# Performance work log

Hardware: AMD Instinct MI355X
Metric: run time of the kernel (lower is better)

The kernel has to match this reference:

```python
import jax, jax.numpy as jnp
import numpy as np

EPSILON = 0.1
ALPHA = 0.5
N_ITER = 10
B, N, D, N_USERS = 4096, 4096, 16, 100000


def setup_inputs() -> dict:
    key = jax.random.key(0)
    k1, k2, k3, k4, k5, k6 = jax.random.split(key, 6)
    users_tensor = jax.random.randint(k1, (B,), 0, N_USERS)
    pois_tensor = jax.random.randint(k2, (B, N), 0, N)
    D_tensor = jax.random.uniform(k3, (B, N), dtype=jnp.float32)
    # ScaledEmbedding: normal init scaled by 1/embedding_dim
    poi_emb = jax.random.normal(k4, (N, D), dtype=jnp.float32) / D
    user_emb = jax.random.normal(k5, (N_USERS, D), dtype=jnp.float32) / D
    capacities = jax.random.uniform(k6, (N,), dtype=jnp.float32) + 0.5
    return {"users_tensor": users_tensor, "pois_tensor": pois_tensor,
            "D_tensor": D_tensor, "poi_emb": poi_emb,
            "user_emb": user_emb, "capacities": capacities}


def reference(users_tensor, pois_tensor, D_tensor, poi_emb, user_emb, capacities):
    pe = poi_emb[pois_tensor]            # [B, N, D]
    ue = user_emb[users_tensor]          # [B, D]
    dot = jnp.einsum('bnd,bd->bn', pe, ue)   # [B, N]
    affinity = (1.0 - ALPHA) * dot - ALPHA * (D_tensor / jnp.mean(D_tensor))
    K = jnp.exp(affinity / EPSILON)      # [B, N]
    a = jnp.ones((B,), dtype=K.dtype)
    b = capacities

    def body(i, uv):
        u, v = uv
        u = a / (K @ v)        # [B]
        v = b / (K.T @ u)      # [N]
        return (u, v)

    u0 = jnp.ones((B,), dtype=K.dtype)
    v0 = jnp.ones((N,), dtype=K.dtype)
    u, v = jax.lax.fori_loop(0, N_ITER, body, (u0, v0))
    P = K * (u[:, None] * v[None, :])    # [B, N]
    return P
```

## Files before the change

### kernel.cpp

```cpp
#include <hip/hip_runtime.h>
#include <hip/hip_fp16.h>

#define BB 4096
#define NN 4096
#define RPB 4
#define RPI 8
#define NBLK (BB / RPI)

__device__ __forceinline__ int swz(int bid) { return (bid & 7) * 64 + (bid >> 3); }

__global__ __launch_bounds__(256) void k_mean(
        const float* __restrict__ Dt, float* __restrict__ dsum,
        float* __restrict__ v) {
    const int tid = blockIdx.x * blockDim.x + threadIdx.x;
    const int gs = gridDim.x * blockDim.x;
    if (tid < NN) v[tid] = 1.0f;
    const float4* D4 = (const float4*)Dt;
    const int total4 = (BB * NN) / 4;
    float s = 0.f;
    for (int i = tid; i < total4; i += gs) {
        float4 d = D4[i];
        s += (d.x + d.y) + (d.z + d.w);
    }
    #pragma unroll
    for (int off = 32; off > 0; off >>= 1) s += __shfl_down(s, off, 64);
    __shared__ float ls[4];
    if ((threadIdx.x & 63) == 0) ls[threadIdx.x >> 6] = s;
    __syncthreads();
    if (threadIdx.x == 0) atomicAdd(dsum, (ls[0] + ls[1]) + (ls[2] + ls[3]));
}

__global__ __launch_bounds__(256) void k_K(
        const int* __restrict__ users, const int* __restrict__ pois,
        const float* __restrict__ Dt, const float* __restrict__ poi_emb,
        const float* __restrict__ user_emb, const float* __restrict__ dsum,
        __half* __restrict__ K) {
    __shared__ __half slut[RPB][NN];
    __shared__ float ues[RPB * 16];
    const int t = threadIdx.x;
    const int b0 = blockIdx.x * RPB;
    if (t < RPB * 16) {
        int r = t >> 4, d = t & 15;
        ues[t] = user_emb[(size_t)users[b0 + r] * 16 + d];
    }
    __syncthreads();
    float ue[RPB][16];
    #pragma unroll
    for (int r = 0; r < RPB; r++)
        #pragma unroll
        for (int d = 0; d < 16; d++) ue[r][d] = ues[r * 16 + d];

    const float4* pe4 = (const float4*)poi_emb;
    for (int j = t; j < NN; j += 256) {
        float4 p0 = pe4[j * 4 + 0];
        float4 p1 = pe4[j * 4 + 1];
        float4 p2 = pe4[j * 4 + 2];
        float4 p3 = pe4[j * 4 + 3];
        #pragma unroll
        for (int r = 0; r < RPB; r++) {
            float acc = p0.x*ue[r][0]  + p0.y*ue[r][1]  + p0.z*ue[r][2]  + p0.w*ue[r][3]
                      + p1.x*ue[r][4]  + p1.y*ue[r][5]  + p1.z*ue[r][6]  + p1.w*ue[r][7]
                      + p2.x*ue[r][8]  + p2.y*ue[r][9]  + p2.z*ue[r][10] + p2.w*ue[r][11]
                      + p3.x*ue[r][12] + p3.y*ue[r][13] + p3.z*ue[r][14] + p3.w*ue[r][15];
            slut[r][j] = __float2half(acc);
        }
    }
    __syncthreads();
    const float cc = 5.0f * 16777216.0f / dsum[0];
    #pragma unroll
    for (int r = 0; r < RPB; r++) {
        const size_t base = (size_t)(b0 + r) * NN;
        const int4*   p4 = (const int4*)(pois + base);
        const float4* d4 = (const float4*)(Dt + base);
        #pragma unroll
        for (int i = 0; i < NN / 4 / 256; i++) {
            const int q = t + i * 256;
            int4   ci = p4[q];
            float4 cd = d4[q];
            float k0 = __expf(5.0f * __half2float(slut[r][ci.x]) - cc * cd.x);
            float k1 = __expf(5.0f * __half2float(slut[r][ci.y]) - cc * cd.y);
            float k2 = __expf(5.0f * __half2float(slut[r][ci.z]) - cc * cd.z);
            float k3 = __expf(5.0f * __half2float(slut[r][ci.w]) - cc * cd.w);
            __half2* kw = (__half2*)&K[base + 4 * (size_t)q];
            kw[0] = __floats2half2_rn(k0, k1);
            kw[1] = __floats2half2_rn(k2, k3);
        }
    }
}

__global__ __launch_bounds__(512) void k_it(
        const __half* __restrict__ K, const float* __restrict__ v,
        float* __restrict__ part, float* __restrict__ u) {
    const int t = threadIdx.x;
    const int sb = swz(blockIdx.x);
    const int r0 = sb * RPI;

    const float4* w4 = (const float4*)v;
    float4 w0 = w4[2 * t], w1 = w4[2 * t + 1];

    float4 h[RPI];
    #pragma unroll
    for (int r = 0; r < RPI; r++)
        h[r] = ((const float4*)(K + (size_t)(r0 + r) * NN))[t];

    float acc[RPI];
    #pragma unroll
    for (int r = 0; r < RPI; r++) {
        const __half2* a = (const __half2*)&h[r];
        float2 f; float s = 0.f;
        f = __half22float2(a[0]); s += f.x * w0.x + f.y * w0.y;
        f = __half22float2(a[1]); s += f.x * w0.z + f.y * w0.w;
        f = __half22float2(a[2]); s += f.x * w1.x + f.y * w1.y;
        f = __half22float2(a[3]); s += f.x * w1.z + f.y * w1.w;
        acc[r] = s;
    }
    #pragma unroll
    for (int off = 32; off > 0; off >>= 1)
        #pragma unroll
        for (int r = 0; r < RPI; r++) acc[r] += __shfl_down(acc[r], off, 64);
    __shared__ float ls[8][RPI];
    __shared__ float us[RPI];
    if ((t & 63) == 0)
        #pragma unroll
        for (int r = 0; r < RPI; r++) ls[t >> 6][r] = acc[r];
    __syncthreads();
    if (t < RPI) {
        float s = 0.f;
        #pragma unroll
        for (int wv = 0; wv < 8; wv++) s += ls[wv][t];
        float uu = 1.0f / s;
        us[t] = uu;
        u[r0 + t] = uu;
    }
    __syncthreads();

    float4 A0 = make_float4(0, 0, 0, 0), A1 = A0;
    #pragma unroll
    for (int r = 0; r < RPI; r++) {
        const float ur = us[r];
        const __half2* a = (const __half2*)&h[r];
        float2 f;
        f = __half22float2(a[0]); A0.x += ur * f.x; A0.y += ur * f.y;
        f = __half22float2(a[1]); A0.z += ur * f.x; A0.w += ur * f.y;
        f = __half22float2(a[2]); A1.x += ur * f.x; A1.y += ur * f.y;
        f = __half22float2(a[3]); A1.z += ur * f.x; A1.w += ur * f.y;
    }
    float4* p4 = (float4*)(part + (size_t)sb * NN);
    p4[2 * t]     = A0;
    p4[2 * t + 1] = A1;
}

__global__ __launch_bounds__(256) void k_red(
        const float* __restrict__ part, const float* __restrict__ cap,
        float* __restrict__ v) {
    const int t = threadIdx.x;
    const int g = blockIdx.x;
    const int j = t & 7;
    const int s = t >> 3;
    const float4* p4 = (const float4*)part;
    float4 a = make_float4(0, 0, 0, 0);
    #pragma unroll
    for (int i = 0; i < NBLK / 32; i++) {
        float4 x = p4[(size_t)(s + 32 * i) * (NN / 4) + g * 8 + j];
        a.x += x.x; a.y += x.y; a.z += x.z; a.w += x.w;
    }
    __shared__ float4 red[32][8];
    red[s][j] = a;
    __syncthreads();
    if (t < 8) {
        float4 b = red[0][t];
        #pragma unroll
        for (int s2 = 1; s2 < 32; s2++) {
            float4 x = red[s2][t];
            b.x += x.x; b.y += x.y; b.z += x.z; b.w += x.w;
        }
        float4 cc = ((const float4*)cap)[g * 8 + t];
        ((float4*)v)[g * 8 + t] =
            make_float4(cc.x / b.x, cc.y / b.y, cc.z / b.z, cc.w / b.w);
    }
}

__global__ __launch_bounds__(256) void k_P(
        const __half* __restrict__ K, const float* __restrict__ u,
        const float* __restrict__ v, float* __restrict__ P) {
    const int t = threadIdx.x;
    const int sb = swz(blockIdx.x);
    const int r0 = sb * RPI;
    const float4* v4 = (const float4*)v;
    float4 va0 = v4[2 * t],       va1 = v4[2 * t + 1];
    float4 vb0 = v4[512 + 2 * t], vb1 = v4[512 + 2 * t + 1];
    #pragma unroll 2
    for (int r = 0; r < RPI; r++) {
        const int b = r0 + r;
        const float ub = u[b];
        const size_t base = (size_t)b * NN;
        const float4* k4 = (const float4*)(K + base);
        float4 raw0 = k4[t], raw1 = k4[256 + t];
        const __half2* ha = (const __half2*)&raw0;
        const __half2* hb = (const __half2*)&raw1;
        float2 f0 = __half22float2(ha[0]);
        float2 f1 = __half22float2(ha[1]);
        float2 f2 = __half22float2(ha[2]);
        float2 f3 = __half22float2(ha[3]);
        float2 g0 = __half22float2(hb[0]);
        float2 g1 = __half22float2(hb[1]);
        float2 g2 = __half22float2(hb[2]);
        float2 g3 = __half22float2(hb[3]);
        float4* P4 = (float4*)(P + base);
        P4[2*t]       = make_float4(f0.x*ub*va0.x, f0.y*ub*va0.y, f1.x*ub*va0.z, f1.y*ub*va0.w);
        P4[2*t+1]     = make_float4(f2.x*ub*va1.x, f2.y*ub*va1.y, f3.x*ub*va1.z, f3.y*ub*va1.w);
        P4[512+2*t]   = make_float4(g0.x*ub*vb0.x, g0.y*ub*vb0.y, g1.x*ub*vb0.z, g1.y*ub*vb0.w);
        P4[512+2*t+1] = make_float4(g2.x*ub*vb1.x, g2.y*ub*vb1.y, g3.x*ub*vb1.z, g3.y*ub*vb1.w);
    }
}

extern "C" void kernel_launch(void* const* d_in, const int* in_sizes, int n_in,
                              void* d_out, int out_size, void* d_ws, size_t ws_size,
                              hipStream_t stream) {
    const int*   users    = (const int*)d_in[0];
    const int*   pois     = (const int*)d_in[1];
    const float* Dt       = (const float*)d_in[2];
    const float* poi_emb  = (const float*)d_in[3];
    const float* user_emb = (const float*)d_in[4];
    const float* cap      = (const float*)d_in[5];
    float* out = (float*)d_out;

    float*  wsf  = (float*)d_ws;
    float*  dsum = wsf;
    float*  u    = wsf + 64;
    float*  v    = wsf + 64 + BB;
    __half* Kh   = (__half*)(wsf + 64 + BB + NN);
    float*  part = (float*)d_out;

    hipMemsetAsync(dsum, 0, sizeof(float), stream);
    k_mean<<<2048, 256, 0, stream>>>(Dt, dsum, v);
    k_K<<<BB / RPB, 256, 0, stream>>>(users, pois, Dt, poi_emb, user_emb, dsum, Kh);
    for (int it = 0; it < 10; it++) {
        k_it<<<NBLK, 512, 0, stream>>>(Kh, v, part, u);
        k_red<<<128, 256, 0, stream>>>(part, cap, v);
    }
    k_P<<<NBLK, 256, 0, stream>>>(Kh, u, v, out);
}
```

Measured before the change: 386.6 us.

## Halve rows per K block, batch gather loads, widen column reduction grid

k_K now handles 2 rows per block instead of 4, doubling the grid. It issues all pois/D loads for both rows before computing exponentials, and makes the user-embedding values wave-uniform with readfirstlane. k_red switches from float4 per thread with 128 blocks to scalar columns with 512 blocks and shuffle reductions, spreading the per-iteration column sum over more CUs. The aim is more parallelism and latency hiding, at the cost of recomputing the POI LUT twice as often and using narrower loads in the reduction.

Result: slower. 427.2 us (+10.5%).

```diff
diff --git a/kernel.cpp b/kernel.cpp
--- a/kernel.cpp
+++ b/kernel.cpp
@@ -3,11 +3,15 @@
 
 #define BB 4096
 #define NN 4096
-#define RPB 4
+#define RPB 2
 #define RPI 8
 #define NBLK (BB / RPI)
 
 __device__ __forceinline__ int swz(int bid) { return (bid & 7) * 64 + (bid >> 3); }
+
+__device__ __forceinline__ float rfl(float x) {
+    return __int_as_float(__builtin_amdgcn_readfirstlane(__float_as_int(x)));
+}
 
 __global__ __launch_bounds__(256) void k_mean(
         const float* __restrict__ Dt, float* __restrict__ dsum,
@@ -36,19 +40,19 @@
         const float* __restrict__ user_emb, const float* __restrict__ dsum,
         __half* __restrict__ K) {
     __shared__ __half slut[RPB][NN];
-    __shared__ float ues[RPB * 16];
+    __shared__ float ues_s[RPB * 16];
     const int t = threadIdx.x;
     const int b0 = blockIdx.x * RPB;
     if (t < RPB * 16) {
         int r = t >> 4, d = t & 15;
-        ues[t] = user_emb[(size_t)users[b0 + r] * 16 + d];
+        ues_s[t] = user_emb[(size_t)users[b0 + r] * 16 + d];
     }
     __syncthreads();
     float ue[RPB][16];
     #pragma unroll
     for (int r = 0; r < RPB; r++)
         #pragma unroll
-        for (int d = 0; d < 16; d++) ue[r][d] = ues[r * 16 + d];
+        for (int d = 0; d < 16; d++) ue[r][d] = rfl(ues_s[r * 16 + d]);
 
     const float4* pe4 = (const float4*)poi_emb;
     for (int j = t; j < NN; j += 256) {
@@ -67,24 +71,27 @@
     }
     __syncthreads();
     const float cc = 5.0f * 16777216.0f / dsum[0];
-    #pragma unroll
-    for (int r = 0; r < RPB; r++) {
-        const size_t base = (size_t)(b0 + r) * NN;
-        const int4*   p4 = (const int4*)(pois + base);
-        const float4* d4 = (const float4*)(Dt + base);
-        #pragma unroll
-        for (int i = 0; i < NN / 4 / 256; i++) {
-            const int q = t + i * 256;
-            int4   ci = p4[q];
-            float4 cd = d4[q];
-            float k0 = __expf(5.0f * __half2float(slut[r][ci.x]) - cc * cd.x);
-            float k1 = __expf(5.0f * __half2float(slut[r][ci.y]) - cc * cd.y);
-            float k2 = __expf(5.0f * __half2float(slut[r][ci.z]) - cc * cd.z);
-            float k3 = __expf(5.0f * __half2float(slut[r][ci.w]) - cc * cd.w);
-            __half2* kw = (__half2*)&K[base + 4 * (size_t)q];
-            kw[0] = __floats2half2_rn(k0, k1);
-            kw[1] = __floats2half2_rn(k2, k3);
-        }
+
+    const int4*   pA = (const int4*)(pois + (size_t)b0 * NN);
+    const float4* dA = (const float4*)(Dt + (size_t)b0 * NN);
+    const int4*   pB = (const int4*)(pois + (size_t)(b0 + 1) * NN);
+    const float4* dB = (const float4*)(Dt + (size_t)(b0 + 1) * NN);
+    int4 ci[8]; float4 cd[8];
+    #pragma unroll
+    for (int i = 0; i < 4; i++) { ci[i] = pA[t + i * 256]; cd[i] = dA[t + i * 256]; }
+    #pragma unroll
+    for (int i = 0; i < 4; i++) { ci[4+i] = pB[t + i * 256]; cd[4+i] = dB[t + i * 256]; }
+    #pragma unroll
+    for (int s = 0; s < 8; s++) {
+        const int r = s >> 2;
+        const int q = t + (s & 3) * 256;
+        float k0 = __expf(5.0f * __half2float(slut[r][ci[s].x]) - cc * cd[s].x);
+        float k1 = __expf(5.0f * __half2float(slut[r][ci[s].y]) - cc * cd[s].y);
+        float k2 = __expf(5.0f * __half2float(slut[r][ci[s].z]) - cc * cd[s].z);
+        float k3 = __expf(5.0f * __half2float(slut[r][ci[s].w]) - cc * cd[s].w);
+        __half2* kw = (__half2*)&K[(size_t)(b0 + r) * NN + 4 * (size_t)q];
+        kw[0] = __floats2half2_rn(k0, k1);
+        kw[1] = __floats2half2_rn(k2, k3);
     }
 }
 
@@ -155,28 +162,22 @@
         float* __restrict__ v) {
     const int t = threadIdx.x;
     const int g = blockIdx.x;
-    const int j = t & 7;
-    const int s = t >> 3;
-    const float4* p4 = (const float4*)part;
-    float4 a = make_float4(0, 0, 0, 0);
-    #pragma unroll
-    for (int i = 0; i < NBLK / 32; i++) {
-        float4 x = p4[(size_t)(s + 32 * i) * (NN / 4) + g * 8 + j];
-        a.x += x.x; a.y += x.y; a.z += x.z; a.w += x.w;
-    }
-    __shared__ float4 red[32][8];
-    red[s][j] = a;
+    const int c = t & 7;
+    const int s0 = t >> 3;
+    const float* base = part + 8 * g + c;
+    float a = 0.f;
+    #pragma unroll
+    for (int i = 0; i < NBLK / 32; i++)
+        a += base[(size_t)(s0 + 32 * i) * NN];
+    a += __shfl_down(a, 32, 64);
+    a += __shfl_down(a, 16, 64);
+    a += __shfl_down(a, 8, 64);
+    __shared__ float red[4][8];
+    if ((t & 63) < 8) red[t >> 6][c] = a;
     __syncthreads();
     if (t < 8) {
-        float4 b = red[0][t];
-        #pragma unroll
-        for (int s2 = 1; s2 < 32; s2++) {
-            float4 x = red[s2][t];
-            b.x += x.x; b.y += x.y; b.z += x.z; b.w += x.w;
-        }
-        float4 cc = ((const float4*)cap)[g * 8 + t];
-        ((float4*)v)[g * 8 + t] =
-            make_float4(cc.x / b.x, cc.y / b.y, cc.z / b.z, cc.w / b.w);
+        float s = (red[0][t] + red[1][t]) + (red[2][t] + red[3][t]);
+        v[8 * g + t] = cap[8 * g + t] / s;
     }
 }
 
@@ -232,12 +233,12 @@
     __half* Kh   = (__half*)(wsf + 64 + BB + NN);
     float*  part = (float*)d_out;
 
-    hipMemsetAsync(dsum, 0, sizeof(float), stream);
+    (void)hipMemsetAsync(dsum, 0, sizeof(float), stream);
     k_mean<<<2048, 256, 0, stream>>>(Dt, dsum, v);
     k_K<<<BB / RPB, 256, 0, stream>>>(users, pois, Dt, poi_emb, user_emb, dsum, Kh);
     for (int it = 0; it < 10; it++) {
         k_it<<<NBLK, 512, 0, stream>>>(Kh, v, part, u);
-        k_red<<<128, 256, 0, stream>>>(part, cap, v);
+        k_red<<<512, 256, 0, stream>>>(part, cap, v);
     }
     k_P<<<NBLK, 256, 0, stream>>>(Kh, u, v, out);
 }
```

## Fuse column reduction into Sinkhorn iteration kernel with ping-pong partial buffers

Applied to the files above, without the earlier changes.

Removes the separate k_red launch per iteration. Each k_it block now first reduces all 64 column-partial slices and divides capacities by the sums to rebuild v itself, then processes 64 rows in chunks of 8. A final k_fin kernel computes v once for the output pass, and k_K gets a block swizzle. This halves the kernel launches in the loop, but the grid drops to 64 blocks, each doing serialized chunk work with barriers. Every block also re-reads the full 1 MB partial buffer each iteration, which risks poor bandwidth use across the GPU.

Measured after the change: 558.7 us. 44.5% more time.

```diff
diff --git a/kernel.cpp b/kernel.cpp
--- a/kernel.cpp
+++ b/kernel.cpp
@@ -4,17 +4,24 @@
 #define BB 4096
 #define NN 4096
 #define RPB 4
-#define RPI 8
-#define NBLK (BB / RPI)
-
-__device__ __forceinline__ int swz(int bid) { return (bid & 7) * 64 + (bid >> 3); }
+#define IBLK 64
+#define IROW (BB / IBLK)
+#define ICH 8
+#define NSL IBLK
+#define RPP 8
+#define PBLK (BB / RPP)
+
+__device__ __forceinline__ int swzK(int bid) { return (bid & 7) * 128 + (bid >> 3); }
+__device__ __forceinline__ int swzI(int bid) { return (bid & 7) * 8   + (bid >> 3); }
+__device__ __forceinline__ int swzP(int bid) { return (bid & 7) * 64  + (bid >> 3); }
 
 __global__ __launch_bounds__(256) void k_mean(
         const float* __restrict__ Dt, float* __restrict__ dsum,
-        float* __restrict__ v) {
+        float* __restrict__ partA, const float* __restrict__ cap) {
     const int tid = blockIdx.x * blockDim.x + threadIdx.x;
     const int gs = gridDim.x * blockDim.x;
-    if (tid < NN) v[tid] = 1.0f;
+    for (int i = tid; i < NSL * NN; i += gs)
+        partA[i] = (i < NN) ? cap[i] : 0.f;
     const float4* D4 = (const float4*)Dt;
     const int total4 = (BB * NN) / 4;
     float s = 0.f;
@@ -38,7 +45,7 @@
     __shared__ __half slut[RPB][NN];
     __shared__ float ues[RPB * 16];
     const int t = threadIdx.x;
-    const int b0 = blockIdx.x * RPB;
+    const int b0 = swzK(blockIdx.x) * RPB;
     if (t < RPB * 16) {
         int r = t >> 4, d = t & 15;
         ues[t] = user_emb[(size_t)users[b0 + r] * 16 + d];
@@ -89,108 +96,103 @@
 }
 
 __global__ __launch_bounds__(512) void k_it(
-        const __half* __restrict__ K, const float* __restrict__ v,
-        float* __restrict__ part, float* __restrict__ u) {
+        const __half* __restrict__ K, const float* __restrict__ cap,
+        const float* __restrict__ partIn, float* __restrict__ partOut,
+        float* __restrict__ u) {
     const int t = threadIdx.x;
-    const int sb = swz(blockIdx.x);
-    const int r0 = sb * RPI;
-
-    const float4* w4 = (const float4*)v;
-    float4 w0 = w4[2 * t], w1 = w4[2 * t + 1];
-
-    float4 h[RPI];
-    #pragma unroll
-    for (int r = 0; r < RPI; r++)
-        h[r] = ((const float4*)(K + (size_t)(r0 + r) * NN))[t];
-
-    float acc[RPI];
-    #pragma unroll
-    for (int r = 0; r < RPI; r++) {
-        const __half2* a = (const __half2*)&h[r];
-        float2 f; float s = 0.f;
-        f = __half22float2(a[0]); s += f.x * w0.x + f.y * w0.y;
-        f = __half22float2(a[1]); s += f.x * w0.z + f.y * w0.w;
-        f = __half22float2(a[2]); s += f.x * w1.x + f.y * w1.y;
-        f = __half22float2(a[3]); s += f.x * w1.z + f.y * w1.w;
-        acc[r] = s;
-    }
-    #pragma unroll
-    for (int off = 32; off > 0; off >>= 1)
-        #pragma unroll
-        for (int r = 0; r < RPI; r++) acc[r] += __shfl_down(acc[r], off, 64);
-    __shared__ float ls[8][RPI];
-    __shared__ float us[RPI];
-    if ((t & 63) == 0)
-        #pragma unroll
-        for (int r = 0; r < RPI; r++) ls[t >> 6][r] = acc[r];
-    __syncthreads();
-    if (t < RPI) {
-        float s = 0.f;
-        #pragma unroll
-        for (int wv = 0; wv < 8; wv++) s += ls[wv][t];
-        float uu = 1.0f / s;
-        us[t] = uu;
-        u[r0 + t] = uu;
-    }
-    __syncthreads();
-
+    const int sb = swzI(blockIdx.x);
+    const int r0 = sb * IROW;
+
+    const float4* p4 = (const float4*)partIn;
+    float4 d0 = make_float4(0, 0, 0, 0), d1 = d0;
+    #pragma unroll 8
+    for (int s = 0; s < NSL; s++) {
+        float4 x0 = p4[s * (NN / 4) + 2 * t];
+        float4 x1 = p4[s * (NN / 4) + 2 * t + 1];
+        d0.x += x0.x; d0.y += x0.y; d0.z += x0.z; d0.w += x0.w;
+        d1.x += x1.x; d1.y += x1.y; d1.z += x1.z; d1.w += x1.w;
+    }
+    float4 c0 = ((const float4*)cap)[2 * t], c1 = ((const float4*)cap)[2 * t + 1];
+    float4 w0 = make_float4(c0.x / d0.x, c0.y / d0.y, c0.z / d0.z, c0.w / d0.w);
+    float4 w1 = make_float4(c1.x / d1.x, c1.y / d1.y, c1.z / d1.z, c1.w / d1.w);
+
+    __shared__ float ls[8][ICH];
+    __shared__ float us[ICH];
     float4 A0 = make_float4(0, 0, 0, 0), A1 = A0;
-    #pragma unroll
-    for (int r = 0; r < RPI; r++) {
-        const float ur = us[r];
-        const __half2* a = (const __half2*)&h[r];
-        float2 f;
-        f = __half22float2(a[0]); A0.x += ur * f.x; A0.y += ur * f.y;
-        f = __half22float2(a[1]); A0.z += ur * f.x; A0.w += ur * f.y;
-        f = __half22float2(a[2]); A1.x += ur * f.x; A1.y += ur * f.y;
-        f = __half22float2(a[3]); A1.z += ur * f.x; A1.w += ur * f.y;
-    }
-    float4* p4 = (float4*)(part + (size_t)sb * NN);
-    p4[2 * t]     = A0;
-    p4[2 * t + 1] = A1;
-}
-
-__global__ __launch_bounds__(256) void k_red(
+
+    #pragma unroll 1
+    for (int ch = 0; ch < IROW / ICH; ch++) {
+        const int rr = r0 + ch * ICH;
+        float4 h[ICH];
+        #pragma unroll
+        for (int r = 0; r < ICH; r++)
+            h[r] = ((const float4*)(K + (size_t)(rr + r) * NN))[t];
+        float acc[ICH];
+        #pragma unroll
+        for (int r = 0; r < ICH; r++) {
+            const __half2* a = (const __half2*)&h[r];
+            float2 f; float s = 0.f;
+            f = __half22float2(a[0]); s += f.x * w0.x + f.y * w0.y;
+            f = __half22float2(a[1]); s += f.x * w0.z + f.y * w0.w;
+            f = __half22float2(a[2]); s += f.x * w1.x + f.y * w1.y;
+            f = __half22float2(a[3]); s += f.x * w1.z + f.y * w1.w;
+            acc[r] = s;
+        }
+        #pragma unroll
+        for (int off = 32; off > 0; off >>= 1)
+            #pragma unroll
+            for (int r = 0; r < ICH; r++) acc[r] += __shfl_down(acc[r], off, 64);
+        __syncthreads();
+        if ((t & 63) == 0)
+            #pragma unroll
+            for (int r = 0; r < ICH; r++) ls[t >> 6][r] = acc[r];
+        __syncthreads();
+        if (t < ICH) {
+            float s = 0.f;
+            #pragma unroll
+            for (int wv = 0; wv < 8; wv++) s += ls[wv][t];
+            float uu = 1.0f / s;
+            us[t] = uu;
+            u[rr + t] = uu;
+        }
+        __syncthreads();
+        #pragma unroll
+        for (int r = 0; r < ICH; r++) {
+            const float ur = us[r];
+            const __half2* a = (const __half2*)&h[r];
+            float2 f;
+            f = __half22float2(a[0]); A0.x += ur * f.x; A0.y += ur * f.y;
+            f = __half22float2(a[1]); A0.z += ur * f.x; A0.w += ur * f.y;
+            f = __half22float2(a[2]); A1.x += ur * f.x; A1.y += ur * f.y;
+            f = __half22float2(a[3]); A1.z += ur * f.x; A1.w += ur * f.y;
+        }
+    }
+    float4* o4 = (float4*)partOut + (size_t)sb * (NN / 4);
+    o4[2 * t]     = A0;
+    o4[2 * t + 1] = A1;
+}
+
+__global__ __launch_bounds__(512) void k_fin(
         const float* __restrict__ part, const float* __restrict__ cap,
         float* __restrict__ v) {
-    const int t = threadIdx.x;
-    const int g = blockIdx.x;
-    const int j = t & 7;
-    const int s = t >> 3;
-    const float4* p4 = (const float4*)part;
-    float4 a = make_float4(0, 0, 0, 0);
-    #pragma unroll
-    for (int i = 0; i < NBLK / 32; i++) {
-        float4 x = p4[(size_t)(s + 32 * i) * (NN / 4) + g * 8 + j];
-        a.x += x.x; a.y += x.y; a.z += x.z; a.w += x.w;
-    }
-    __shared__ float4 red[32][8];
-    red[s][j] = a;
-    __syncthreads();
-    if (t < 8) {
-        float4 b = red[0][t];
-        #pragma unroll
-        for (int s2 = 1; s2 < 32; s2++) {
-            float4 x = red[s2][t];
-            b.x += x.x; b.y += x.y; b.z += x.z; b.w += x.w;
-        }
-        float4 cc = ((const float4*)cap)[g * 8 + t];
-        ((float4*)v)[g * 8 + t] =
-            make_float4(cc.x / b.x, cc.y / b.y, cc.z / b.z, cc.w / b.w);
-    }
+    const int c = blockIdx.x * 512 + threadIdx.x;
+    float s = 0.f;
+    #pragma unroll 8
+    for (int sl = 0; sl < NSL; sl++) s += part[sl * NN + c];
+    v[c] = cap[c] / s;
 }
 
 __global__ __launch_bounds__(256) void k_P(
         const __half* __restrict__ K, const float* __restrict__ u,
         const float* __restrict__ v, float* __restrict__ P) {
     const int t = threadIdx.x;
-    const int sb = swz(blockIdx.x);
-    const int r0 = sb * RPI;
+    const int sb = swzP(blockIdx.x);
+    const int r0 = sb * RPP;
     const float4* v4 = (const float4*)v;
     float4 va0 = v4[2 * t],       va1 = v4[2 * t + 1];
     float4 vb0 = v4[512 + 2 * t], vb1 = v4[512 + 2 * t + 1];
     #pragma unroll 2
-    for (int r = 0; r < RPI; r++) {
+    for (int r = 0; r < RPP; r++) {
         const int b = r0 + r;
         const float ub = u[b];
         const size_t base = (size_t)b * NN;
@@ -230,14 +232,17 @@
     float*  u    = wsf + 64;
     float*  v    = wsf + 64 + BB;
     __half* Kh   = (__half*)(wsf + 64 + BB + NN);
-    float*  part = (float*)d_out;
-
-    hipMemsetAsync(dsum, 0, sizeof(float), stream);
-    k_mean<<<2048, 256, 0, stream>>>(Dt, dsum, v);
+    float*  partA = (float*)d_out;
+    float*  partB = partA + NSL * NN;
+
+    (void)hipMemsetAsync(dsum, 0, sizeof(float), stream);
+    k_mean<<<2048, 256, 0, stream>>>(Dt, dsum, partA, cap);
     k_K<<<BB / RPB, 256, 0, stream>>>(users, pois, Dt, poi_emb, user_emb, dsum, Kh);
     for (int it = 0; it < 10; it++) {
-        k_it<<<NBLK, 512, 0, stream>>>(Kh, v, part, u);
-        k_red<<<128, 256, 0, stream>>>(part, cap, v);
-    }
-    k_P<<<NBLK, 256, 0, stream>>>(Kh, u, v, out);
-}
+        const float* pin  = (it & 1) ? partB : partA;
+        float*       pout = (it & 1) ? partA : partB;
+        k_it<<<IBLK, 512, 0, stream>>>(Kh, cap, pin, pout, u);
+    }
+    k_fin<<<NN / 512, 512, 0, stream>>>(partA, cap, v);
+    k_P<<<PBLK, 256, 0, stream>>>(Kh, u, v, out);
+}
```

## Use nontemporal loads/stores to keep K resident in cache across iterations

Applied to the files above, without the earlier changes.

Streaming-only data (D, pois, partial sums, the final P output, and part of K) now uses nontemporal loads and stores so it does not evict the fp16 K matrix from the last-level cache. Only K blocks whose slot index is at or above a threshold are loaded nontemporally, so the rest of K can stay cached across the ten Sinkhorn iterations. k_K gets a block swizzle as well. The risk is that a wrong threshold or cache-policy behaviour raises DRAM traffic instead.

Result: faster. 372.0 us (-3.8%).

```diff
diff --git a/kernel.cpp b/kernel.cpp
--- a/kernel.cpp
+++ b/kernel.cpp
@@ -6,8 +6,23 @@
 #define RPB 4
 #define RPI 8
 #define NBLK (BB / RPI)
-
-__device__ __forceinline__ int swz(int bid) { return (bid & 7) * 64 + (bid >> 3); }
+#define NTSLOT 60
+
+__device__ __forceinline__ int swzK(int bid) { return (bid & 7) * 128 + (bid >> 3); }
+
+typedef float vf4 __attribute__((ext_vector_type(4)));
+typedef int   vi4 __attribute__((ext_vector_type(4)));
+__device__ __forceinline__ float4 ntl4(const float4* p) {
+    vf4 r = __builtin_nontemporal_load((const vf4*)p);
+    return *(float4*)&r;
+}
+__device__ __forceinline__ int4 ntl4i(const int4* p) {
+    vi4 r = __builtin_nontemporal_load((const vi4*)p);
+    return *(int4*)&r;
+}
+__device__ __forceinline__ void nts4(float4* p, float4 v) {
+    __builtin_nontemporal_store(*(vf4*)&v, (vf4*)p);
+}
 
 __global__ __launch_bounds__(256) void k_mean(
         const float* __restrict__ Dt, float* __restrict__ dsum,
@@ -19,7 +34,7 @@
     const int total4 = (BB * NN) / 4;
     float s = 0.f;
     for (int i = tid; i < total4; i += gs) {
-        float4 d = D4[i];
+        float4 d = ntl4(&D4[i]);
         s += (d.x + d.y) + (d.z + d.w);
     }
     #pragma unroll
@@ -38,7 +53,7 @@
     __shared__ __half slut[RPB][NN];
     __shared__ float ues[RPB * 16];
     const int t = threadIdx.x;
-    const int b0 = blockIdx.x * RPB;
+    const int b0 = swzK(blockIdx.x) * RPB;
     if (t < RPB * 16) {
         int r = t >> 4, d = t & 15;
         ues[t] = user_emb[(size_t)users[b0 + r] * 16 + d];
@@ -75,8 +90,8 @@
         #pragma unroll
         for (int i = 0; i < NN / 4 / 256; i++) {
             const int q = t + i * 256;
-            int4   ci = p4[q];
-            float4 cd = d4[q];
+            int4   ci = ntl4i(&p4[q]);
+            float4 cd = ntl4(&d4[q]);
             float k0 = __expf(5.0f * __half2float(slut[r][ci.x]) - cc * cd.x);
             float k1 = __expf(5.0f * __half2float(slut[r][ci.y]) - cc * cd.y);
             float k2 = __expf(5.0f * __half2float(slut[r][ci.z]) - cc * cd.z);
@@ -92,16 +107,20 @@
         const __half* __restrict__ K, const float* __restrict__ v,
         float* __restrict__ part, float* __restrict__ u) {
     const int t = threadIdx.x;
-    const int sb = swz(blockIdx.x);
+    const int slot = blockIdx.x >> 3;
+    const int sb = (blockIdx.x & 7) * 64 + slot;
     const int r0 = sb * RPI;
+    const bool nt = (slot >= NTSLOT);
 
     const float4* w4 = (const float4*)v;
     float4 w0 = w4[2 * t], w1 = w4[2 * t + 1];
 
     float4 h[RPI];
     #pragma unroll
-    for (int r = 0; r < RPI; r++)
-        h[r] = ((const float4*)(K + (size_t)(r0 + r) * NN))[t];
+    for (int r = 0; r < RPI; r++) {
+        const float4* p = (const float4*)(K + (size_t)(r0 + r) * NN) + t;
+        h[r] = nt ? ntl4(p) : *p;
+    }
 
     float acc[RPI];
     #pragma unroll
@@ -146,8 +165,8 @@
         f = __half22float2(a[3]); A1.z += ur * f.x; A1.w += ur * f.y;
     }
     float4* p4 = (float4*)(part + (size_t)sb * NN);
-    p4[2 * t]     = A0;
-    p4[2 * t + 1] = A1;
+    nts4(&p4[2 * t],     A0);
+    nts4(&p4[2 * t + 1], A1);
 }
 
 __global__ __launch_bounds__(256) void k_red(
@@ -161,7 +180,7 @@
     float4 a = make_float4(0, 0, 0, 0);
     #pragma unroll
     for (int i = 0; i < NBLK / 32; i++) {
-        float4 x = p4[(size_t)(s + 32 * i) * (NN / 4) + g * 8 + j];
+        float4 x = ntl4(&p4[(size_t)(s + 32 * i) * (NN / 4) + g * 8 + j]);
         a.x += x.x; a.y += x.y; a.z += x.z; a.w += x.w;
     }
     __shared__ float4 red[32][8];
@@ -184,8 +203,10 @@
         const __half* __restrict__ K, const float* __restrict__ u,
         const float* __restrict__ v, float* __restrict__ P) {
     const int t = threadIdx.x;
-    const int sb = swz(blockIdx.x);
+    const int slot = blockIdx.x >> 3;
+    const int sb = (blockIdx.x & 7) * 64 + slot;
     const int r0 = sb * RPI;
+    const bool nt = (slot >= NTSLOT);
     const float4* v4 = (const float4*)v;
     float4 va0 = v4[2 * t],       va1 = v4[2 * t + 1];
     float4 vb0 = v4[512 + 2 * t], vb1 = v4[512 + 2 * t + 1];
@@ -195,7 +216,8 @@
         const float ub = u[b];
         const size_t base = (size_t)b * NN;
         const float4* k4 = (const float4*)(K + base);
-        float4 raw0 = k4[t], raw1 = k4[256 + t];
+        float4 raw0 = nt ? ntl4(&k4[t])       : k4[t];
+        float4 raw1 = nt ? ntl4(&k4[256 + t]) : k4[256 + t];
         const __half2* ha = (const __half2*)&raw0;
         const __half2* hb = (const __half2*)&raw1;
         float2 f0 = __half22float2(ha[0]);
@@ -207,10 +229,10 @@
         float2 g2 = __half22float2(hb[2]);
         float2 g3 = __half22float2(hb[3]);
         float4* P4 = (float4*)(P + base);
-        P4[2*t]       = make_float4(f0.x*ub*va0.x, f0.y*ub*va0.y, f1.x*ub*va0.z, f1.y*ub*va0.w);
-        P4[2*t+1]     = make_float4(f2.x*ub*va1.x, f2.y*ub*va1.y, f3.x*ub*va1.z, f3.y*ub*va1.w);
-        P4[512+2*t]   = make_float4(g0.x*ub*vb0.x, g0.y*ub*vb0.y, g1.x*ub*vb0.z, g1.y*ub*vb0.w);
-        P4[512+2*t+1] = make_float4(g2.x*ub*vb1.x, g2.y*ub*vb1.y, g3.x*ub*vb1.z, g3.y*ub*vb1.w);
+        nts4(&P4[2*t],       make_float4(f0.x*ub*va0.x, f0.y*ub*va0.y, f1.x*ub*va0.z, f1.y*ub*va0.w));
+        nts4(&P4[2*t+1],     make_float4(f2.x*ub*va1.x, f2.y*ub*va1.y, f3.x*ub*va1.z, f3.y*ub*va1.w));
+        nts4(&P4[512+2*t],   make_float4(g0.x*ub*vb0.x, g0.y*ub*vb0.y, g1.x*ub*vb0.z, g1.y*ub*vb0.w));
+        nts4(&P4[512+2*t+1], make_float4(g2.x*ub*vb1.x, g2.y*ub*vb1.y, g3.x*ub*vb1.z, g3.y*ub*vb1.w));
     }
 }
 
@@ -232,7 +254,7 @@
     __half* Kh   = (__half*)(wsf + 64 + BB + NN);
     float*  part = (float*)d_out;
 
-    hipMemsetAsync(dsum, 0, sizeof(float), stream);
+    (void)hipMemsetAsync(dsum, 0, sizeof(float), stream);
     k_mean<<<2048, 256, 0, stream>>>(Dt, dsum, v);
     k_K<<<BB / RPB, 256, 0, stream>>>(users, pois, Dt, poi_emb, user_emb, dsum, Kh);
     for (int it = 0; it < 10; it++) {
```
